# Optimization experiments

Hardware: AMD Instinct MI355X
Metric: run time of the kernel (lower is better)

Reference implementation:

```python
import jax, jax.numpy as jnp
import numpy as np

L, S, N, E, H = 1024, 2048, 4, 512, 8
HD = E // H
LN_EPS = 1e-5


def embed_rotary(x, cos, sin):
    # x, cos, sin: (N, T, E). Rotates interleaved even/odd feature pairs.
    x2 = jnp.stack([-x[..., 1::2], x[..., ::2]], axis=-1).reshape(x.shape)
    return x * cos + x2 * sin


def setup_inputs() -> dict:
    key = jax.random.key(0)
    ks = jax.random.split(key, 8)
    query = jax.random.normal(ks[0], (L, N, E), jnp.float32)
    value = jax.random.normal(ks[1], (S, N, E), jnp.float32)
    # rotary PE tables: [..., 0] = cos, [..., 1] = sin of per-position angles
    qa = jax.random.uniform(ks[2], (N, L, E), jnp.float32, 0.0, 2.0 * np.pi)
    ka = jax.random.uniform(ks[3], (N, S, E), jnp.float32, 0.0, 2.0 * np.pi)
    query_pos = jnp.stack([jnp.cos(qa), jnp.sin(qa)], axis=-1)
    value_pos = jnp.stack([jnp.cos(ka), jnp.sin(ka)], axis=-1)
    w_scale = 1.0 / np.sqrt(E)
    in_proj_weight = jax.random.normal(ks[4], (3 * E, E), jnp.float32) * w_scale
    in_proj_bias = jnp.zeros((3 * E,), jnp.float32)
    out_proj_weight = jax.random.normal(ks[5], (E, E), jnp.float32) * w_scale
    out_proj_bias = jnp.zeros((E,), jnp.float32)
    ln_gamma = jnp.ones((E,), jnp.float32)
    ln_beta = jnp.zeros((E,), jnp.float32)
    return {
        'query': query, 'value': value,
        'query_pos': query_pos, 'value_pos': value_pos,
        'in_proj_weight': in_proj_weight, 'in_proj_bias': in_proj_bias,
        'out_proj_weight': out_proj_weight, 'out_proj_bias': out_proj_bias,
        'ln_gamma': ln_gamma, 'ln_beta': ln_beta,
    }


def reference(query, value, query_pos, value_pos,
              in_proj_weight, in_proj_bias,
              out_proj_weight, out_proj_bias,
              ln_gamma, ln_beta):
    Lq, Nb, Em = query.shape
    scaling = (Em // H) ** -0.5
    # kv_same path of the custom MHA: q from W[:E], (k, v) from W[E:] chunked
    q = query @ in_proj_weight[:Em].T + in_proj_bias[:Em]
    kv = value @ in_proj_weight[Em:].T + in_proj_bias[Em:]
    k, v = kv[..., :Em], kv[..., Em:]
    q = q * scaling
    # rotary PE (applied batch-first, then back to (L, N, E))
    q = embed_rotary(q.transpose(1, 0, 2), query_pos[..., 0], query_pos[..., 1]).transpose(1, 0, 2)
    k = embed_rotary(k.transpose(1, 0, 2), value_pos[..., 0], value_pos[..., 1]).transpose(1, 0, 2)
    # (L, N, E) -> (N, H, L, HD), matching torch view(L, N*H, HD).transpose(0, 1)
    qh = q.reshape(Lq, Nb, H, HD).transpose(1, 2, 0, 3)
    kh = k.reshape(-1, Nb, H, HD).transpose(1, 2, 0, 3)
    vh = v.reshape(-1, Nb, H, HD).transpose(1, 2, 0, 3)
    attn = jax.nn.softmax(jnp.einsum('nhld,nhsd->nhls', qh, kh), axis=-1)
    out = jnp.einsum('nhls,nhsd->nhld', attn, vh)  # (N, H, L, HD)
    out = out.transpose(2, 0, 1, 3).reshape(Lq, Nb, Em)
    out = out @ out_proj_weight.T + out_proj_bias
    # residual + LayerNorm
    y = query + out
    mu = jnp.mean(y, axis=-1, keepdims=True)
    var = jnp.mean(jnp.square(y - mu), axis=-1, keepdims=True)
    y = (y - mu) / jnp.sqrt(var + LN_EPS) * ln_gamma + ln_beta
    return y
```

## Files before the change

### kernel.cpp

```cpp
#include <hip/hip_runtime.h>
#include <math.h>

#define L_  1024
#define S_  2048
#define NB  4
#define E_  512
#define H_  8
#define HD_ 64
#define SPLIT 2

constexpr float SCALING = 0.125f;
constexpr float LNEPS   = 1e-5f;

typedef __attribute__((ext_vector_type(8))) short s16x8;
typedef __attribute__((ext_vector_type(8))) unsigned short u16x8;
typedef __attribute__((ext_vector_type(4))) float f32x4;
typedef unsigned short ushort_t;

__device__ __forceinline__ unsigned short f2bf(float f) {
    unsigned u = __builtin_bit_cast(unsigned, f);
    u += 0x7fffu + ((u >> 16) & 1u);
    return (unsigned short)(u >> 16);
}
__device__ __forceinline__ float bf2f(unsigned short h) {
    unsigned u = ((unsigned)h) << 16;
    return __builtin_bit_cast(float, u);
}
__device__ __forceinline__ unsigned packbf(float a, float b) {
    return (unsigned)f2bf(a) | ((unsigned)f2bf(b) << 16);
}

__global__ __launch_bounds__(256)
void cast4_kernel(const float* __restrict__ s0, const float* __restrict__ s1,
                  const float* __restrict__ s2, const float* __restrict__ s3,
                  ushort_t* __restrict__ d0, ushort_t* __restrict__ d1,
                  ushort_t* __restrict__ d2, ushort_t* __restrict__ d3,
                  int c0, int c1, int c2, int c3)
{
    int i = blockIdx.x * 256 + threadIdx.x;
    const float* s; ushort_t* d; int off;
    if      (i < c0) { s = s0; d = d0; off = i; }
    else if (i < c1) { s = s1; d = d1; off = i - c0; }
    else if (i < c2) { s = s2; d = d2; off = i - c1; }
    else if (i < c3) { s = s3; d = d3; off = i - c2; }
    else return;
    const float4* sp = (const float4*)(s + (size_t)off * 8);
    float4 a = sp[0], b = sp[1];
    u16x8 o;
    o[0] = f2bf(a.x); o[1] = f2bf(a.y); o[2] = f2bf(a.z); o[3] = f2bf(a.w);
    o[4] = f2bf(b.x); o[5] = f2bf(b.y); o[6] = f2bf(b.z); o[7] = f2bf(b.w);
    *(u16x8*)(d + (size_t)off * 8) = o;
}

template<int MR, int EPI>
__global__ __launch_bounds__(256)
void gemm_bf16_kernel(const ushort_t* __restrict__ A,
                      const ushort_t* __restrict__ Bw,
                      ushort_t* __restrict__ Cb,
                      const float* __restrict__ bias,
                      const float* __restrict__ resid,
                      float* __restrict__ Y,
                      int nfeat)
{
    constexpr int BM = MR * 32;
    __shared__ ushort_t As[BM * 32];
    __shared__ ushort_t Bs[128 * 32];
    const int t = threadIdx.x;
    const int w = t >> 6, l = t & 63;
    const int wr = w >> 1, wc = w & 1;
    const int g = l >> 4, c16 = l & 15;
    const int m0 = blockIdx.y * BM;
    const int n0 = blockIdx.x * 128;

    f32x4 acc[MR][4];
    #pragma unroll
    for (int m = 0; m < MR; ++m)
        #pragma unroll
        for (int n = 0; n < 4; ++n) acc[m][n] = (f32x4){0.f, 0.f, 0.f, 0.f};

    for (int k0 = 0; k0 < 512; k0 += 32) {
        #pragma unroll
        for (int ch = t; ch < BM * 4; ch += 256) {
            int r = ch >> 2, c = ch & 3;
            s16x8 v = *(const s16x8*)(A + (size_t)(m0 + r) * 512 + k0 + c * 8);
            int cp = c ^ ((r >> 1) & 3);
            *(s16x8*)((char*)As + r * 64 + cp * 16) = v;
        }
        #pragma unroll
        for (int ch = t; ch < 512; ch += 256) {
            int r = ch >> 2, c = ch & 3;
            s16x8 v = *(const s16x8*)(Bw + (size_t)(n0 + r) * 512 + k0 + c * 8);
            int cp = c ^ ((r >> 1) & 3);
            *(s16x8*)((char*)Bs + r * 64 + cp * 16) = v;
        }
        __syncthreads();
        s16x8 fa[MR], fb[4];
        #pragma unroll
        for (int m = 0; m < MR; ++m) {
            int r = wr * (MR * 16) + m * 16 + c16;
            fa[m] = *(const s16x8*)((char*)As + r * 64 + ((g ^ ((r >> 1) & 3)) * 16));
        }
        #pragma unroll
        for (int n = 0; n < 4; ++n) {
            int r = wc * 64 + n * 16 + c16;
            fb[n] = *(const s16x8*)((char*)Bs + r * 64 + ((g ^ ((r >> 1) & 3)) * 16));
        }
        #pragma unroll
        for (int m = 0; m < MR; ++m)
            #pragma unroll
            for (int n = 0; n < 4; ++n)
                acc[m][n] = __builtin_amdgcn_mfma_f32_16x16x32_bf16(fa[m], fb[n], acc[m][n], 0, 0, 0);
        __syncthreads();
    }

    #pragma unroll
    for (int m = 0; m < MR; ++m) {
        #pragma unroll
        for (int n = 0; n < 4; ++n) {
            int col = n0 + wc * 64 + n * 16 + c16;
            #pragma unroll
            for (int r = 0; r < 4; ++r) {
                int row = m0 + wr * (MR * 16) + m * 16 + g * 4 + r;
                if (EPI == 0) {
                    Cb[(size_t)row * nfeat + col] = f2bf(acc[m][n][r]);
                } else {
                    float v = acc[m][n][r] + bias[col] + resid[(size_t)row * 512 + col];
                    Y[(size_t)row * 512 + col] = v;
                }
            }
        }
    }
}

__global__ __launch_bounds__(256)
void epi_q_kernel(const ushort_t* __restrict__ Cq,
                  const float* __restrict__ bias,
                  const float* __restrict__ qpos,
                  ushort_t* __restrict__ qrot)
{
    int tid = blockIdx.x * 256 + threadIdx.x;
    int token = tid >> 6;
    int fo = (tid & 63) * 8;
    int lq = token >> 2, n = token & 3;
    u16x8 cv = *(const u16x8*)(Cq + (size_t)token * 512 + fo);
    const float4* bp = (const float4*)(bias + fo);
    float4 b0 = bp[0], b1 = bp[1];
    float x[8];
    x[0] = (bf2f(cv[0]) + b0.x) * SCALING; x[1] = (bf2f(cv[1]) + b0.y) * SCALING;
    x[2] = (bf2f(cv[2]) + b0.z) * SCALING; x[3] = (bf2f(cv[3]) + b0.w) * SCALING;
    x[4] = (bf2f(cv[4]) + b1.x) * SCALING; x[5] = (bf2f(cv[5]) + b1.y) * SCALING;
    x[6] = (bf2f(cv[6]) + b1.z) * SCALING; x[7] = (bf2f(cv[7]) + b1.w) * SCALING;
    const float* pp = qpos + ((size_t)(n * L_ + lq) * 512 + fo) * 2;
    u16x8 o;
    #pragma unroll
    for (int jp = 0; jp < 4; ++jp) {
        float4 p = *(const float4*)(pp + jp * 4);
        float v0 = x[2 * jp], v1 = x[2 * jp + 1];
        o[2 * jp]     = f2bf(v0 * p.x - v1 * p.y);
        o[2 * jp + 1] = f2bf(v1 * p.z + v0 * p.w);
    }
    int h = fo >> 6, hd = fo & 63;
    *(u16x8*)(qrot + ((size_t)((n * H_ + h) * L_ + lq)) * HD_ + hd) = o;
}

__global__ __launch_bounds__(256)
void epi_kv_kernel(const ushort_t* __restrict__ Ckv,
                   const float* __restrict__ bias,
                   const float* __restrict__ vpos,
                   ushort_t* __restrict__ krot,
                   ushort_t* __restrict__ vperm)
{
    int tid = blockIdx.x * 256 + threadIdx.x;
    int token = tid >> 7;
    int fo = (tid & 127) * 8;
    int s = token >> 2, n = token & 3;
    u16x8 cv = *(const u16x8*)(Ckv + (size_t)token * 1024 + fo);
    const float4* bp = (const float4*)(bias + fo);
    float4 b0 = bp[0], b1 = bp[1];
    float x[8];
    x[0] = bf2f(cv[0]) + b0.x; x[1] = bf2f(cv[1]) + b0.y;
    x[2] = bf2f(cv[2]) + b0.z; x[3] = bf2f(cv[3]) + b0.w;
    x[4] = bf2f(cv[4]) + b1.x; x[5] = bf2f(cv[5]) + b1.y;
    x[6] = bf2f(cv[6]) + b1.z; x[7] = bf2f(cv[7]) + b1.w;
    u16x8 o;
    if (fo < 512) {
        const float* pp = vpos + ((size_t)(n * S_ + s) * 512 + fo) * 2;
        #pragma unroll
        for (int jp = 0; jp < 4; ++jp) {
            float4 p = *(const float4*)(pp + jp * 4);
            float v0 = x[2 * jp], v1 = x[2 * jp + 1];
            o[2 * jp]     = f2bf(v0 * p.x - v1 * p.y);
            o[2 * jp + 1] = f2bf(v1 * p.z + v0 * p.w);
        }
        int h = fo >> 6, hd = fo & 63;
        *(u16x8*)(krot + ((size_t)((n * H_ + h) * S_ + s)) * HD_ + hd) = o;
    } else {
        #pragma unroll
        for (int j = 0; j < 8; ++j) o[j] = f2bf(x[j]);
        int f = fo - 512;
        int h = f >> 6, hd = f & 63;
        *(u16x8*)(vperm + ((size_t)((n * H_ + h) * S_ + s)) * HD_ + hd) = o;
    }
}

__global__ __launch_bounds__(256)
void vtrans_kernel(const ushort_t* __restrict__ vin,
                   ushort_t* __restrict__ vout)
{
    __shared__ ushort_t T[64][68];
    const int t  = threadIdx.x;
    const int s0 = blockIdx.x * 64;
    const int h  = blockIdx.y, n = blockIdx.z;
    const ushort_t* src = vin + (size_t)((n * H_ + h) * S_ + s0) * HD_;
    #pragma unroll
    for (int p = 0; p < 4; ++p) {
        int e = p * 1024 + t * 4;
        int row = e >> 6, col = e & 63;
        *(ushort4*)&T[row][col] = *(const ushort4*)(src + row * HD_ + col);
    }
    __syncthreads();
    ushort_t* dst = vout + (size_t)(n * H_ + h) * HD_ * S_ + s0;
    #pragma unroll
    for (int p = 0; p < 4; ++p) {
        int d  = p * 16 + (t >> 4);
        int sc = (t & 15) * 4;
        ushort4 o;
        o.x = T[sc + 0][d]; o.y = T[sc + 1][d]; o.z = T[sc + 2][d]; o.w = T[sc + 3][d];
        *(ushort4*)(dst + (size_t)d * S_ + sc) = o;
    }
}

__global__ __launch_bounds__(256)
void attn_mfma_kernel(const ushort_t* __restrict__ qg,
                      const ushort_t* __restrict__ kg,
                      const ushort_t* __restrict__ vtg,
                      float* __restrict__ pctx,
                      float2* __restrict__ pml)
{
    __shared__ __align__(16) char smem[40960];
    char* Kb0 = smem;
    char* Kb1 = smem + 8192;
    char* Vb0 = smem + 16384;
    char* Vb1 = smem + 24576;
    const int t = threadIdx.x;
    const int w = t >> 6, l = t & 63;
    char* Ps = smem + 32768 + w * 2048;
    const int g = l >> 4, c16 = l & 15;
    const int h = blockIdx.y;
    const int n = blockIdx.z / SPLIT, sp = blockIdx.z % SPLIT;
    const int qb0 = blockIdx.x * 64;
    constexpr int NT = (S_ / SPLIT) / 64;

    const char* kbase  = (const char*)(kg  + (size_t)(n * H_ + h) * S_ * HD_)
                       + (size_t)sp * (S_ / SPLIT) * 128;
    const char* vtbase = (const char*)(vtg + (size_t)(n * H_ + h) * HD_ * S_)
                       + (size_t)sp * (S_ / SPLIT) * 2;

    const int qgl = qb0 + w * 16 + c16;
    const char* qrow = (const char*)(qg + (size_t)((n * H_ + h) * L_ + qgl) * HD_);
    s16x8 qf0 = *(const s16x8*)(qrow + 16 * g);
    s16x8 qf1 = *(const s16x8*)(qrow + 64 + 16 * g);

    const int srow = t >> 3;
    const int scol = (t & 7) * 16;

    float mrun = -1e30f, lrun = 0.f;
    f32x4 oacc[4];
    #pragma unroll
    for (int s2 = 0; s2 < 4; ++s2) oacc[s2] = (f32x4){0.f, 0.f, 0.f, 0.f};

    uint4 kreg[2], vreg[2];
    #pragma unroll
    for (int c = 0; c < 2; ++c) {
        int row = c * 32 + srow;
        kreg[c] = *(const uint4*)(kbase  + (size_t)row * 128 + scol);
        vreg[c] = *(const uint4*)(vtbase + (size_t)row * (S_ * 2) + scol);
    }
    #pragma unroll
    for (int c = 0; c < 2; ++c) {
        int row = c * 32 + srow;
        int sw  = scol ^ ((row & 7) << 4);
        *(uint4*)(Kb0 + row * 128 + sw) = kreg[c];
        *(uint4*)(Vb0 + row * 128 + sw) = vreg[c];
    }
    __syncthreads();

    int cur = 0;
    for (int st = 0; st < NT; ++st) {
        if (st + 1 < NT) {
            const char* kP = kbase  + (size_t)(st + 1) * 64 * 128;
            const char* vP = vtbase + (size_t)(st + 1) * 128;
            #pragma unroll
            for (int c = 0; c < 2; ++c) {
                int row = c * 32 + srow;
                kreg[c] = *(const uint4*)(kP + (size_t)row * 128 + scol);
                vreg[c] = *(const uint4*)(vP + (size_t)row * (S_ * 2) + scol);
            }
        }
        char* K = cur ? Kb1 : Kb0;
        char* V = cur ? Vb1 : Vb0;

        f32x4 sacc[4];
        #pragma unroll
        for (int sub = 0; sub < 4; ++sub) {
            int row = sub * 16 + c16;
            int x = (row & 7) << 4;
            s16x8 kf0 = *(const s16x8*)(K + row * 128 + ((16 * g) ^ x));
            s16x8 kf1 = *(const s16x8*)(K + row * 128 + ((64 + 16 * g) ^ x));
            f32x4 z = (f32x4){0.f, 0.f, 0.f, 0.f};
            z = __builtin_amdgcn_mfma_f32_16x16x32_bf16(kf0, qf0, z, 0, 0, 0);
            z = __builtin_amdgcn_mfma_f32_16x16x32_bf16(kf1, qf1, z, 0, 0, 0);
            sacc[sub] = z;
        }

        float mloc = sacc[0][0];
        #pragma unroll
        for (int sub = 0; sub < 4; ++sub)
            #pragma unroll
            for (int r = 0; r < 4; ++r) mloc = fmaxf(mloc, sacc[sub][r]);
        mloc = fmaxf(mloc, __shfl_xor(mloc, 16, 64));
        mloc = fmaxf(mloc, __shfl_xor(mloc, 32, 64));
        float mnew = fmaxf(mrun, mloc);
        float scl = __expf(mrun - mnew);
        mrun = mnew;

        float p[4][4];
        float ps = 0.f;
        #pragma unroll
        for (int sub = 0; sub < 4; ++sub)
            #pragma unroll
            for (int r = 0; r < 4; ++r) {
                float e = __expf(sacc[sub][r] - mnew);
                p[sub][r] = e;
                ps += e;
            }
        ps += __shfl_xor(ps, 16, 64);
        ps += __shfl_xor(ps, 32, 64);
        lrun = lrun * scl + ps;

        #pragma unroll
        for (int sub = 0; sub < 4; ++sub) {
            uint2 pk;
            pk.x = packbf(p[sub][0], p[sub][1]);
            pk.y = packbf(p[sub][2], p[sub][3]);
            int by = (32 * sub + 8 * g) ^ ((c16 & 7) << 4);
            *(uint2*)(Ps + c16 * 128 + by) = pk;
        }

        float sclr[4];
        #pragma unroll
        for (int r = 0; r < 4; ++r) sclr[r] = __shfl(scl, 4 * g + r, 16);
        #pragma unroll
        for (int s2 = 0; s2 < 4; ++s2)
            #pragma unroll
            for (int r = 0; r < 4; ++r) oacc[s2][r] *= sclr[r];

        #pragma unroll
        for (int sh = 0; sh < 2; ++sh) {
            s16x8 pf = *(const s16x8*)(Ps + c16 * 128 + ((64 * sh + 16 * g) ^ ((c16 & 7) << 4)));
            #pragma unroll
            for (int s2 = 0; s2 < 4; ++s2) {
                int row = s2 * 16 + c16;
                int x = (row & 7) << 4;
                s16x8 vf = *(const s16x8*)(V + row * 128 + ((64 * sh + 16 * g) ^ x));
                oacc[s2] = __builtin_amdgcn_mfma_f32_16x16x32_bf16(pf, vf, oacc[s2], 0, 0, 0);
            }
        }

        if (st + 1 < NT) {
            char* Kn = cur ? Kb0 : Kb1;
            char* Vn = cur ? Vb0 : Vb1;
            #pragma unroll
            for (int c = 0; c < 2; ++c) {
                int row = c * 32 + srow;
                int sw  = scol ^ ((row & 7) << 4);
                *(uint4*)(Kn + row * 128 + sw) = kreg[c];
                *(uint4*)(Vn + row * 128 + sw) = vreg[c];
            }
            __syncthreads();
            cur ^= 1;
        }
    }

    float* pc = pctx + (size_t)sp * (L_ * NB * E_);
    #pragma unroll
    for (int r = 0; r < 4; ++r) {
        int q = qb0 + w * 16 + 4 * g + r;
        #pragma unroll
        for (int s2 = 0; s2 < 4; ++s2) {
            pc[((size_t)q * NB + n) * E_ + h * HD_ + s2 * 16 + c16] = oacc[s2][r];
        }
    }
    if (g == 0) {
        pml[(((size_t)sp * NB + n) * H_ + h) * L_ + qgl] = make_float2(mrun, lrun);
    }
}

__global__ __launch_bounds__(256)
void attn_combine_kernel(const float* __restrict__ pctx,
                         const float2* __restrict__ pml,
                         ushort_t* __restrict__ ctxb)
{
    int idx = blockIdx.x * 256 + threadIdx.x;
    int h  = (idx >> 6) & 7;
    int tq = idx >> 9;
    int q = tq >> 2, n = tq & 3;
    float O0 = pctx[idx];
    float O1 = pctx[(size_t)(L_ * NB * E_) + idx];
    float2 ml0 = pml[(((size_t)0 * NB + n) * H_ + h) * L_ + q];
    float2 ml1 = pml[(((size_t)1 * NB + n) * H_ + h) * L_ + q];
    float ms = fmaxf(ml0.x, ml1.x);
    float a0 = __expf(ml0.x - ms), a1 = __expf(ml1.x - ms);
    float num = O0 * a0 + O1 * a1;
    float den = ml0.y * a0 + ml1.y * a1;
    ctxb[idx] = f2bf(num / den);
}

__global__ __launch_bounds__(256)
void ln_kernel(float* __restrict__ y, const float* __restrict__ gamma,
               const float* __restrict__ beta)
{
    __shared__ float red1[4], red2[4];
    const int row = blockIdx.x;
    const int t   = threadIdx.x;
    float* p = y + (size_t)row * E_;
    float x0 = p[t], x1 = p[t + 256];

    float s = x0 + x1;
    #pragma unroll
    for (int o = 32; o >= 1; o >>= 1) s += __shfl_down(s, o, 64);
    if ((t & 63) == 0) red1[t >> 6] = s;
    __syncthreads();
    const float mu = (red1[0] + red1[1] + red1[2] + red1[3]) * (1.0f / E_);

    const float d0 = x0 - mu, d1 = x1 - mu;
    float vs = d0 * d0 + d1 * d1;
    #pragma unroll
    for (int o = 32; o >= 1; o >>= 1) vs += __shfl_down(vs, o, 64);
    if ((t & 63) == 0) red2[t >> 6] = vs;
    __syncthreads();
    const float var  = (red2[0] + red2[1] + red2[2] + red2[3]) * (1.0f / E_);
    const float rstd = rsqrtf(var + LNEPS);

    p[t]       = d0 * rstd * gamma[t]       + beta[t];
    p[t + 256] = d1 * rstd * gamma[t + 256] + beta[t + 256];
}

extern "C" void kernel_launch(void* const* d_in, const int* in_sizes, int n_in,
                              void* d_out, int out_size, void* d_ws, size_t ws_size,
                              hipStream_t stream) {
    const float* query = (const float*)d_in[0];
    const float* value = (const float*)d_in[1];
    const float* qpos  = (const float*)d_in[2];
    const float* vpos  = (const float*)d_in[3];
    const float* ipw   = (const float*)d_in[4];
    const float* ipb   = (const float*)d_in[5];
    const float* opw   = (const float*)d_in[6];
    const float* opb   = (const float*)d_in[7];
    const float* gamma = (const float*)d_in[8];
    const float* beta  = (const float*)d_in[9];
    float* out = (float*)d_out;

    char* ws = (char*)d_ws;
    ushort_t* kvC   = (ushort_t*)(ws);
    ushort_t* vbf   = (ushort_t*)(ws + (16u << 20));
    ushort_t* qbf   = (ushort_t*)(ws + (24u << 20));
    ushort_t* wbf   = (ushort_t*)(ws + (28u << 20));
    ushort_t* obf   = (ushort_t*)(ws + (30u << 20));
    ushort_t* qC    = (ushort_t*)(ws + (31u << 20));
    ushort_t* qrot  = (ushort_t*)(ws + (35u << 20));
    ushort_t* krot  = (ushort_t*)(ws + (39u << 20));
    ushort_t* vperm = (ushort_t*)(ws + (47u << 20));
    ushort_t* vt    = (ushort_t*)(ws);
    ushort_t* ctxb  = (ushort_t*)(ws + (8u << 20));
    float2*   pml   = (float2*)  (ws + (12u << 20));
    float*    pctx  = (float*)   (ws + (13u << 20));

    const int c0 = 262144;
    const int c1 = c0 + 524288;
    const int c2 = c1 + 98304;
    const int c3 = c2 + 32768;
    cast4_kernel<<<3584, 256, 0, stream>>>(query, value, ipw, opw,
                                           qbf, vbf, wbf, obf, c0, c1, c2, c3);

    gemm_bf16_kernel<2, 0><<<dim3(512 / 128, 4096 / 64), 256, 0, stream>>>(
        qbf, wbf, qC, nullptr, nullptr, nullptr, 512);
    gemm_bf16_kernel<4, 0><<<dim3(1024 / 128, 8192 / 128), 256, 0, stream>>>(
        vbf, wbf + (size_t)E_ * E_, kvC, nullptr, nullptr, nullptr, 1024);

    epi_q_kernel<<<1024, 256, 0, stream>>>(qC, ipb, qpos, qrot);
    epi_kv_kernel<<<4096, 256, 0, stream>>>(kvC, ipb + E_, vpos, krot, vperm);

    vtrans_kernel<<<dim3(S_ / 64, H_, NB), 256, 0, stream>>>(vperm, vt);

    attn_mfma_kernel<<<dim3(L_ / 64, H_, NB * SPLIT), 256, 0, stream>>>(
        qrot, krot, vt, pctx, pml);
    attn_combine_kernel<<<(L_ * NB * E_) / 256, 256, 0, stream>>>(pctx, pml, ctxb);

    gemm_bf16_kernel<2, 1><<<dim3(512 / 128, 4096 / 64), 256, 0, stream>>>(
        ctxb, obf, nullptr, opb, query, out, 512);

    ln_kernel<<<L_ * NB, 256, 0, stream>>>(out, gamma, beta);
}
```

Before: 252.6 us.

## Fuse Q/KV projection GEMMs with bias, scaling and rotary epilogue

Replaces the two projection GEMMs and the two epilogue kernels with one kernel that computes both Q and KV tiles in a single grid and applies bias, scaling and rotary embedding directly from the accumulators, exchanging pair partners via lane shuffles. This removes the round trip of the bf16 intermediate C buffers and three kernel launches. In exchange the epilogue writes scalar bf16 values and reads cos/sin with strided, uncoalesced loads, and the KV GEMM now uses the smaller 64-row tile. The partial context buffer is moved to a new workspace offset to avoid overlap.

```diff
diff --git a/kernel.cpp b/kernel.cpp
--- a/kernel.cpp
+++ b/kernel.cpp
@@ -52,6 +52,110 @@
     *(u16x8*)(d + (size_t)off * 8) = o;
 }
 
+__global__ __launch_bounds__(256)
+void qkv_gemm_rope_kernel(const ushort_t* __restrict__ qbf,
+                          const ushort_t* __restrict__ vbf,
+                          const ushort_t* __restrict__ wbf,
+                          const float* __restrict__ ipb,
+                          const float* __restrict__ qpos,
+                          const float* __restrict__ vpos,
+                          ushort_t* __restrict__ qrot,
+                          ushort_t* __restrict__ krot,
+                          ushort_t* __restrict__ vperm)
+{
+    __shared__ ushort_t As[64 * 32];
+    __shared__ ushort_t Bs[128 * 32];
+    const int t = threadIdx.x;
+    const int w = t >> 6, l = t & 63;
+    const int wr = w >> 1, wc = w & 1;
+    const int g = l >> 4, c16 = l & 15;
+
+    const int bid = blockIdx.x;
+    const bool isq = bid < 256;
+    int fb, tb;
+    const ushort_t* Abase;
+    const ushort_t* Wbase;
+    if (isq) { fb = bid & 3;  tb = bid >> 2; Abase = qbf; Wbase = wbf; }
+    else     { int b = bid - 256; fb = b & 7; tb = b >> 3; Abase = vbf; Wbase = wbf + 512 * 512; }
+    const int m0 = tb * 64;
+    const int n0 = fb * 128;
+    const int Ltok = isq ? L_ : S_;
+
+    f32x4 acc[2][4];
+    #pragma unroll
+    for (int m = 0; m < 2; ++m)
+        #pragma unroll
+        for (int n = 0; n < 4; ++n) acc[m][n] = (f32x4){0.f, 0.f, 0.f, 0.f};
+
+    for (int k0 = 0; k0 < 512; k0 += 32) {
+        {
+            int ch = t;
+            int r = ch >> 2, c = ch & 3;
+            s16x8 v = *(const s16x8*)(Abase + (size_t)(m0 + r) * 512 + k0 + c * 8);
+            int cp = c ^ ((r >> 1) & 3);
+            *(s16x8*)((char*)As + r * 64 + cp * 16) = v;
+        }
+        #pragma unroll
+        for (int ch = t; ch < 512; ch += 256) {
+            int r = ch >> 2, c = ch & 3;
+            s16x8 v = *(const s16x8*)(Wbase + (size_t)(n0 + r) * 512 + k0 + c * 8);
+            int cp = c ^ ((r >> 1) & 3);
+            *(s16x8*)((char*)Bs + r * 64 + cp * 16) = v;
+        }
+        __syncthreads();
+        s16x8 fa[2], fb4[4];
+        #pragma unroll
+        for (int m = 0; m < 2; ++m) {
+            int r = wr * 32 + m * 16 + c16;
+            fa[m] = *(const s16x8*)((char*)As + r * 64 + ((g ^ ((r >> 1) & 3)) * 16));
+        }
+        #pragma unroll
+        for (int n = 0; n < 4; ++n) {
+            int r = wc * 64 + n * 16 + c16;
+            fb4[n] = *(const s16x8*)((char*)Bs + r * 64 + ((g ^ ((r >> 1) & 3)) * 16));
+        }
+        #pragma unroll
+        for (int m = 0; m < 2; ++m)
+            #pragma unroll
+            for (int n = 0; n < 4; ++n)
+                acc[m][n] = __builtin_amdgcn_mfma_f32_16x16x32_bf16(fa[m], fb4[n], acc[m][n], 0, 0, 0);
+        __syncthreads();
+    }
+
+    const bool dorot = isq || (n0 < 512);
+    const float sgn = (l & 1) ? 1.f : -1.f;
+    const float* pos = isq ? qpos : vpos;
+    #pragma unroll
+    for (int m = 0; m < 2; ++m) {
+        #pragma unroll
+        for (int nf = 0; nf < 4; ++nf) {
+            const int col = n0 + wc * 64 + nf * 16 + c16;
+            const float bia = ipb[isq ? col : 512 + col];
+            #pragma unroll
+            for (int r = 0; r < 4; ++r) {
+                const int row = m0 + wr * 32 + m * 16 + g * 4 + r;
+                const int tok = row >> 2, n = row & 3;
+                float v = acc[m][nf][r] + bia;
+                if (isq) v *= SCALING;
+                if (dorot) {
+                    float2 cs = *(const float2*)(pos + (((size_t)n * Ltok + tok) * 512 + col) * 2);
+                    float p = __shfl_xor(v, 1, 64);
+                    float o = v * cs.x + sgn * p * cs.y;
+                    const int hh = col >> 6, hd = col & 63;
+                    ushort_t* dst = isq
+                        ? qrot + ((size_t)(n * H_ + hh) * L_ + tok) * HD_ + hd
+                        : krot + ((size_t)(n * H_ + hh) * S_ + tok) * HD_ + hd;
+                    *dst = f2bf(o);
+                } else {
+                    const int e = col - 512;
+                    const int hh = e >> 6, hd = e & 63;
+                    vperm[((size_t)(n * H_ + hh) * S_ + tok) * HD_ + hd] = f2bf(v);
+                }
+            }
+        }
+    }
+}
+
 template<int MR, int EPI>
 __global__ __launch_bounds__(256)
 void gemm_bf16_kernel(const ushort_t* __restrict__ A,
@@ -129,77 +233,6 @@
                 }
             }
         }
-    }
-}
-
-__global__ __launch_bounds__(256)
-void epi_q_kernel(const ushort_t* __restrict__ Cq,
-                  const float* __restrict__ bias,
-                  const float* __restrict__ qpos,
-                  ushort_t* __restrict__ qrot)
-{
-    int tid = blockIdx.x * 256 + threadIdx.x;
-    int token = tid >> 6;
-    int fo = (tid & 63) * 8;
-    int lq = token >> 2, n = token & 3;
-    u16x8 cv = *(const u16x8*)(Cq + (size_t)token * 512 + fo);
-    const float4* bp = (const float4*)(bias + fo);
-    float4 b0 = bp[0], b1 = bp[1];
-    float x[8];
-    x[0] = (bf2f(cv[0]) + b0.x) * SCALING; x[1] = (bf2f(cv[1]) + b0.y) * SCALING;
-    x[2] = (bf2f(cv[2]) + b0.z) * SCALING; x[3] = (bf2f(cv[3]) + b0.w) * SCALING;
-    x[4] = (bf2f(cv[4]) + b1.x) * SCALING; x[5] = (bf2f(cv[5]) + b1.y) * SCALING;
-    x[6] = (bf2f(cv[6]) + b1.z) * SCALING; x[7] = (bf2f(cv[7]) + b1.w) * SCALING;
-    const float* pp = qpos + ((size_t)(n * L_ + lq) * 512 + fo) * 2;
-    u16x8 o;
-    #pragma unroll
-    for (int jp = 0; jp < 4; ++jp) {
-        float4 p = *(const float4*)(pp + jp * 4);
-        float v0 = x[2 * jp], v1 = x[2 * jp + 1];
-        o[2 * jp]     = f2bf(v0 * p.x - v1 * p.y);
-        o[2 * jp + 1] = f2bf(v1 * p.z + v0 * p.w);
-    }
-    int h = fo >> 6, hd = fo & 63;
-    *(u16x8*)(qrot + ((size_t)((n * H_ + h) * L_ + lq)) * HD_ + hd) = o;
-}
-
-__global__ __launch_bounds__(256)
-void epi_kv_kernel(const ushort_t* __restrict__ Ckv,
-                   const float* __restrict__ bias,
-                   const float* __restrict__ vpos,
-                   ushort_t* __restrict__ krot,
-                   ushort_t* __restrict__ vperm)
-{
-    int tid = blockIdx.x * 256 + threadIdx.x;
-    int token = tid >> 7;
-    int fo = (tid & 127) * 8;
-    int s = token >> 2, n = token & 3;
-    u16x8 cv = *(const u16x8*)(Ckv + (size_t)token * 1024 + fo);
-    const float4* bp = (const float4*)(bias + fo);
-    float4 b0 = bp[0], b1 = bp[1];
-    float x[8];
-    x[0] = bf2f(cv[0]) + b0.x; x[1] = bf2f(cv[1]) + b0.y;
-    x[2] = bf2f(cv[2]) + b0.z; x[3] = bf2f(cv[3]) + b0.w;
-    x[4] = bf2f(cv[4]) + b1.x; x[5] = bf2f(cv[5]) + b1.y;
-    x[6] = bf2f(cv[6]) + b1.z; x[7] = bf2f(cv[7]) + b1.w;
-    u16x8 o;
-    if (fo < 512) {
-        const float* pp = vpos + ((size_t)(n * S_ + s) * 512 + fo) * 2;
-        #pragma unroll
-        for (int jp = 0; jp < 4; ++jp) {
-            float4 p = *(const float4*)(pp + jp * 4);
-            float v0 = x[2 * jp], v1 = x[2 * jp + 1];
-            o[2 * jp]     = f2bf(v0 * p.x - v1 * p.y);
-            o[2 * jp + 1] = f2bf(v1 * p.z + v0 * p.w);
-        }
-        int h = fo >> 6, hd = fo & 63;
-        *(u16x8*)(krot + ((size_t)((n * H_ + h) * S_ + s)) * HD_ + hd) = o;
-    } else {
-        #pragma unroll
-        for (int j = 0; j < 8; ++j) o[j] = f2bf(x[j]);
-        int f = fo - 512;
-        int h = f >> 6, hd = f & 63;
-        *(u16x8*)(vperm + ((size_t)((n * H_ + h) * S_ + s)) * HD_ + hd) = o;
     }
 }
 
@@ -462,19 +495,17 @@
     float* out = (float*)d_out;
 
     char* ws = (char*)d_ws;
-    ushort_t* kvC   = (ushort_t*)(ws);
     ushort_t* vbf   = (ushort_t*)(ws + (16u << 20));
     ushort_t* qbf   = (ushort_t*)(ws + (24u << 20));
     ushort_t* wbf   = (ushort_t*)(ws + (28u << 20));
     ushort_t* obf   = (ushort_t*)(ws + (30u << 20));
-    ushort_t* qC    = (ushort_t*)(ws + (31u << 20));
     ushort_t* qrot  = (ushort_t*)(ws + (35u << 20));
     ushort_t* krot  = (ushort_t*)(ws + (39u << 20));
     ushort_t* vperm = (ushort_t*)(ws + (47u << 20));
     ushort_t* vt    = (ushort_t*)(ws);
     ushort_t* ctxb  = (ushort_t*)(ws + (8u << 20));
     float2*   pml   = (float2*)  (ws + (12u << 20));
-    float*    pctx  = (float*)   (ws + (13u << 20));
+    float*    pctx  = (float*)   (ws + (55u << 20));
 
     const int c0 = 262144;
     const int c1 = c0 + 524288;
@@ -483,13 +514,8 @@
     cast4_kernel<<<3584, 256, 0, stream>>>(query, value, ipw, opw,
                                            qbf, vbf, wbf, obf, c0, c1, c2, c3);
 
-    gemm_bf16_kernel<2, 0><<<dim3(512 / 128, 4096 / 64), 256, 0, stream>>>(
-        qbf, wbf, qC, nullptr, nullptr, nullptr, 512);
-    gemm_bf16_kernel<4, 0><<<dim3(1024 / 128, 8192 / 128), 256, 0, stream>>>(
-        vbf, wbf + (size_t)E_ * E_, kvC, nullptr, nullptr, nullptr, 1024);
-
-    epi_q_kernel<<<1024, 256, 0, stream>>>(qC, ipb, qpos, qrot);
-    epi_kv_kernel<<<4096, 256, 0, stream>>>(kvC, ipb + E_, vpos, krot, vperm);
+    qkv_gemm_rope_kernel<<<1280, 256, 0, stream>>>(
+        qbf, vbf, wbf, ipb, qpos, vpos, qrot, krot, vperm);
 
     vtrans_kernel<<<dim3(S_ / 64, H_, NB), 256, 0, stream>>>(vperm, vt);
 
```

Result: slower. 271.4 us (+7.4%).

## Merge Q and KV projection GEMMs, use exp2 softmax with lazy rescaling

Applied to the files above, without the earlier changes.

Replaces the two separate Q and KV projection GEMM launches with one kernel of 640 blocks that picks its operand set from the block index. Folds log2(e) into the query scaling so the softmax, and the combine step, use exp2f instead of __expf. The attention kernel now rescales the output accumulator and running sum only when some lane's running max would grow by more than 8 (the threshold applies to log2-scaled scores), skipping that multiply-and-shuffle work in most tiles. The output-projection GEMM uses a smaller row tile to launch more blocks. Lazy rescaling lets probabilities reach up to 2^8 before renormalisation; this fits within fp32 and bf16 range but slightly changes rounding.

```diff
diff --git a/kernel.cpp b/kernel.cpp
--- a/kernel.cpp
+++ b/kernel.cpp
@@ -10,6 +10,7 @@
 #define SPLIT 2
 
 constexpr float SCALING = 0.125f;
+constexpr float LOG2E   = 1.44269504f;
 constexpr float LNEPS   = 1e-5f;
 
 typedef __attribute__((ext_vector_type(8))) short s16x8;
@@ -52,6 +53,88 @@
     *(u16x8*)(d + (size_t)off * 8) = o;
 }
 
+__global__ __launch_bounds__(256)
+void qkv_gemm_kernel(const ushort_t* __restrict__ qbf,
+                     const ushort_t* __restrict__ vbf,
+                     const ushort_t* __restrict__ wbf,
+                     ushort_t* __restrict__ qC,
+                     ushort_t* __restrict__ kvC)
+{
+    __shared__ ushort_t As[128 * 32];
+    __shared__ ushort_t Bs[128 * 32];
+    const int t = threadIdx.x;
+    const int w = t >> 6, l = t & 63;
+    const int wr = w >> 1, wc = w & 1;
+    const int g = l >> 4, c16 = l & 15;
+
+    const int bid = blockIdx.x;
+    const ushort_t *A, *W;
+    ushort_t* C;
+    int nfeat, m0, n0;
+    if (bid < 128) {
+        A = qbf; W = wbf; C = qC; nfeat = 512;
+        n0 = (bid & 3) * 128; m0 = (bid >> 2) * 128;
+    } else {
+        int b = bid - 128;
+        A = vbf; W = wbf + 512 * 512; C = kvC; nfeat = 1024;
+        n0 = (b & 7) * 128; m0 = (b >> 3) * 128;
+    }
+
+    f32x4 acc[4][4];
+    #pragma unroll
+    for (int m = 0; m < 4; ++m)
+        #pragma unroll
+        for (int n = 0; n < 4; ++n) acc[m][n] = (f32x4){0.f, 0.f, 0.f, 0.f};
+
+    for (int k0 = 0; k0 < 512; k0 += 32) {
+        #pragma unroll
+        for (int ch = t; ch < 512; ch += 256) {
+            int r = ch >> 2, c = ch & 3;
+            s16x8 v = *(const s16x8*)(A + (size_t)(m0 + r) * 512 + k0 + c * 8);
+            int cp = c ^ ((r >> 1) & 3);
+            *(s16x8*)((char*)As + r * 64 + cp * 16) = v;
+        }
+        #pragma unroll
+        for (int ch = t; ch < 512; ch += 256) {
+            int r = ch >> 2, c = ch & 3;
+            s16x8 v = *(const s16x8*)(W + (size_t)(n0 + r) * 512 + k0 + c * 8);
+            int cp = c ^ ((r >> 1) & 3);
+            *(s16x8*)((char*)Bs + r * 64 + cp * 16) = v;
+        }
+        __syncthreads();
+        s16x8 fa[4], fb[4];
+        #pragma unroll
+        for (int m = 0; m < 4; ++m) {
+            int r = wr * 64 + m * 16 + c16;
+            fa[m] = *(const s16x8*)((char*)As + r * 64 + ((g ^ ((r >> 1) & 3)) * 16));
+        }
+        #pragma unroll
+        for (int n = 0; n < 4; ++n) {
+            int r = wc * 64 + n * 16 + c16;
+            fb[n] = *(const s16x8*)((char*)Bs + r * 64 + ((g ^ ((r >> 1) & 3)) * 16));
+        }
+        #pragma unroll
+        for (int m = 0; m < 4; ++m)
+            #pragma unroll
+            for (int n = 0; n < 4; ++n)
+                acc[m][n] = __builtin_amdgcn_mfma_f32_16x16x32_bf16(fa[m], fb[n], acc[m][n], 0, 0, 0);
+        __syncthreads();
+    }
+
+    #pragma unroll
+    for (int m = 0; m < 4; ++m) {
+        #pragma unroll
+        for (int n = 0; n < 4; ++n) {
+            int col = n0 + wc * 64 + n * 16 + c16;
+            #pragma unroll
+            for (int r = 0; r < 4; ++r) {
+                int row = m0 + wr * 64 + m * 16 + g * 4 + r;
+                C[(size_t)row * nfeat + col] = f2bf(acc[m][n][r]);
+            }
+        }
+    }
+}
+
 template<int MR, int EPI>
 __global__ __launch_bounds__(256)
 void gemm_bf16_kernel(const ushort_t* __restrict__ A,
@@ -138,6 +221,7 @@
                   const float* __restrict__ qpos,
                   ushort_t* __restrict__ qrot)
 {
+    const float sc = SCALING * LOG2E;
     int tid = blockIdx.x * 256 + threadIdx.x;
     int token = tid >> 6;
     int fo = (tid & 63) * 8;
@@ -146,10 +230,10 @@
     const float4* bp = (const float4*)(bias + fo);
     float4 b0 = bp[0], b1 = bp[1];
     float x[8];
-    x[0] = (bf2f(cv[0]) + b0.x) * SCALING; x[1] = (bf2f(cv[1]) + b0.y) * SCALING;
-    x[2] = (bf2f(cv[2]) + b0.z) * SCALING; x[3] = (bf2f(cv[3]) + b0.w) * SCALING;
-    x[4] = (bf2f(cv[4]) + b1.x) * SCALING; x[5] = (bf2f(cv[5]) + b1.y) * SCALING;
-    x[6] = (bf2f(cv[6]) + b1.z) * SCALING; x[7] = (bf2f(cv[7]) + b1.w) * SCALING;
+    x[0] = (bf2f(cv[0]) + b0.x) * sc; x[1] = (bf2f(cv[1]) + b0.y) * sc;
+    x[2] = (bf2f(cv[2]) + b0.z) * sc; x[3] = (bf2f(cv[3]) + b0.w) * sc;
+    x[4] = (bf2f(cv[4]) + b1.x) * sc; x[5] = (bf2f(cv[5]) + b1.y) * sc;
+    x[6] = (bf2f(cv[6]) + b1.z) * sc; x[7] = (bf2f(cv[7]) + b1.w) * sc;
     const float* pp = qpos + ((size_t)(n * L_ + lq) * 512 + fo) * 2;
     u16x8 o;
     #pragma unroll
@@ -320,9 +404,20 @@
             for (int r = 0; r < 4; ++r) mloc = fmaxf(mloc, sacc[sub][r]);
         mloc = fmaxf(mloc, __shfl_xor(mloc, 16, 64));
         mloc = fmaxf(mloc, __shfl_xor(mloc, 32, 64));
-        float mnew = fmaxf(mrun, mloc);
-        float scl = __expf(mrun - mnew);
-        mrun = mnew;
+
+        if (!__all(mloc - mrun <= 8.0f)) {
+            float mnew = fmaxf(mrun, mloc);
+            float scl = exp2f(mrun - mnew);
+            float sclr[4];
+            #pragma unroll
+            for (int r = 0; r < 4; ++r) sclr[r] = __shfl(scl, 4 * g + r, 16);
+            #pragma unroll
+            for (int s2 = 0; s2 < 4; ++s2)
+                #pragma unroll
+                for (int r = 0; r < 4; ++r) oacc[s2][r] *= sclr[r];
+            lrun *= scl;
+            mrun = mnew;
+        }
 
         float p[4][4];
         float ps = 0.f;
@@ -330,13 +425,13 @@
         for (int sub = 0; sub < 4; ++sub)
             #pragma unroll
             for (int r = 0; r < 4; ++r) {
-                float e = __expf(sacc[sub][r] - mnew);
+                float e = exp2f(sacc[sub][r] - mrun);
                 p[sub][r] = e;
                 ps += e;
             }
         ps += __shfl_xor(ps, 16, 64);
         ps += __shfl_xor(ps, 32, 64);
-        lrun = lrun * scl + ps;
+        lrun += ps;
 
         #pragma unroll
         for (int sub = 0; sub < 4; ++sub) {
@@ -346,14 +441,6 @@
             int by = (32 * sub + 8 * g) ^ ((c16 & 7) << 4);
             *(uint2*)(Ps + c16 * 128 + by) = pk;
         }
-
-        float sclr[4];
-        #pragma unroll
-        for (int r = 0; r < 4; ++r) sclr[r] = __shfl(scl, 4 * g + r, 16);
-        #pragma unroll
-        for (int s2 = 0; s2 < 4; ++s2)
-            #pragma unroll
-            for (int r = 0; r < 4; ++r) oacc[s2][r] *= sclr[r];
 
         #pragma unroll
         for (int sh = 0; sh < 2; ++sh) {
@@ -410,7 +497,7 @@
     float2 ml0 = pml[(((size_t)0 * NB + n) * H_ + h) * L_ + q];
     float2 ml1 = pml[(((size_t)1 * NB + n) * H_ + h) * L_ + q];
     float ms = fmaxf(ml0.x, ml1.x);
-    float a0 = __expf(ml0.x - ms), a1 = __expf(ml1.x - ms);
+    float a0 = exp2f(ml0.x - ms), a1 = exp2f(ml1.x - ms);
     float num = O0 * a0 + O1 * a1;
     float den = ml0.y * a0 + ml1.y * a1;
     ctxb[idx] = f2bf(num / den);
@@ -483,10 +570,7 @@
     cast4_kernel<<<3584, 256, 0, stream>>>(query, value, ipw, opw,
                                            qbf, vbf, wbf, obf, c0, c1, c2, c3);
 
-    gemm_bf16_kernel<2, 0><<<dim3(512 / 128, 4096 / 64), 256, 0, stream>>>(
-        qbf, wbf, qC, nullptr, nullptr, nullptr, 512);
-    gemm_bf16_kernel<4, 0><<<dim3(1024 / 128, 8192 / 128), 256, 0, stream>>>(
-        vbf, wbf + (size_t)E_ * E_, kvC, nullptr, nullptr, nullptr, 1024);
+    qkv_gemm_kernel<<<640, 256, 0, stream>>>(qbf, vbf, wbf, qC, kvC);
 
     epi_q_kernel<<<1024, 256, 0, stream>>>(qC, ipb, qpos, qrot);
     epi_kv_kernel<<<4096, 256, 0, stream>>>(kvC, ipb + E_, vpos, krot, vperm);
@@ -497,7 +581,7 @@
         qrot, krot, vt, pctx, pml);
     attn_combine_kernel<<<(L_ * NB * E_) / 256, 256, 0, stream>>>(pctx, pml, ctxb);
 
-    gemm_bf16_kernel<2, 1><<<dim3(512 / 128, 4096 / 64), 256, 0, stream>>>(
+    gemm_bf16_kernel<1, 1><<<dim3(512 / 128, 4096 / 32), 256, 0, stream>>>(
         ctxb, obf, nullptr, opb, query, out, 512);
 
     ln_kernel<<<L_ * NB, 256, 0, stream>>>(out, gamma, beta);
```

Result: faster. 235.6 us (-6.7%).
